# Kernel optimization log

Measured on AMD Instinct MI355X. Metric: run time of the kernel, lower is better.

## Reference

```python
import jax, jax.numpy as jnp
import numpy as np

B, S, HID = 2, 1024, 2048
NH, NKV = 32, 8
HD = HID // NH          # 64
N_REP = NH // NKV       # 4
ROPE_BASE = 10000.0


def rope_tables(seq_len, dim):
    inv_freq = 1.0 / (ROPE_BASE ** (np.arange(0, dim, 2, dtype=np.float32) / dim))
    t = jnp.arange(seq_len, dtype=jnp.float32)
    freqs = jnp.outer(t, jnp.asarray(inv_freq))          # [S, HD/2]
    emb = jnp.concatenate([freqs, freqs], axis=-1)       # [S, HD]
    return jnp.cos(emb), jnp.sin(emb)


def rotate_half(x):
    half = x.shape[-1] // 2
    return jnp.concatenate([-x[..., half:], x[..., :half]], axis=-1)


def setup_inputs() -> dict:
    key = jax.random.key(0)
    k1, k2, k3, k4, k5 = jax.random.split(key, 5)
    hidden_states = jax.random.normal(k1, (B, S, HID), dtype=jnp.float32)
    position_ids = jnp.broadcast_to(jnp.arange(S, dtype=jnp.int32), (B, S))
    # additive causal mask [B,1,S,S]: 0 where allowed, large negative where masked
    neg = jnp.finfo(jnp.float32).min
    causal = jnp.tril(jnp.ones((S, S), dtype=bool))
    attention_mask = jnp.where(causal, 0.0, neg)[None, None].astype(jnp.float32)
    attention_mask = jnp.broadcast_to(attention_mask, (B, 1, S, S))
    scale = 0.02
    Wq = jax.random.normal(k2, (HID, NH * HD), dtype=jnp.float32) * scale
    Wk = jax.random.normal(k3, (HID, NKV * HD), dtype=jnp.float32) * scale
    Wv = jax.random.normal(k4, (HID, NKV * HD), dtype=jnp.float32) * scale
    Wo = jax.random.normal(k5, (HID, HID), dtype=jnp.float32) * scale
    return {"hidden_states": hidden_states, "position_ids": position_ids,
            "attention_mask": attention_mask, "Wq": Wq, "Wk": Wk, "Wv": Wv, "Wo": Wo}


def reference(hidden_states, position_ids, attention_mask, Wq, Wk, Wv, Wo):
    b, s, _ = hidden_states.shape
    q = (hidden_states @ Wq).reshape(b, s, NH, HD).transpose(0, 2, 1, 3)    # [b,H,s,d]
    k = (hidden_states @ Wk).reshape(b, s, NKV, HD).transpose(0, 2, 1, 3)   # [b,kv,s,d]
    v = (hidden_states @ Wv).reshape(b, s, NKV, HD).transpose(0, 2, 1, 3)

    cos_t, sin_t = rope_tables(s, HD)                    # [s, d]
    cos = cos_t[position_ids][:, None]                   # [b,1,s,d]
    sin = sin_t[position_ids][:, None]
    q = q * cos + rotate_half(q) * sin
    k = k * cos + rotate_half(k) * sin

    # GQA: repeat each kv head N_REP times along the head axis
    k = jnp.repeat(k, N_REP, axis=1)                     # [b,H,s,d]
    v = jnp.repeat(v, N_REP, axis=1)

    scale = 1.0 / jnp.sqrt(jnp.asarray(HD, dtype=q.dtype))
    scores = jnp.einsum('bhqd,bhkd->bhqk', q, k) * scale
    scores = scores + attention_mask
    scores = jnp.maximum(scores, jnp.finfo(scores.dtype).min)
    w = jax.nn.softmax(scores, axis=-1)
    out = jnp.einsum('bhqk,bhkd->bhqd', w, v)            # [b,H,s,d]
    out = out.transpose(0, 2, 1, 3).reshape(b, s, HID)
    return out @ Wo
```

## Files before the change

kernel.cpp:

```cpp
#include <hip/hip_runtime.h>
#include <hip/hip_bf16.h>
#include <math.h>

constexpr int BB   = 2;
constexpr int SS   = 1024;
constexpr int HID  = 2048;
constexpr int NH   = 32;
constexpr int NKV  = 8;
constexpr int HD   = 64;
constexpr int M    = BB * SS;
constexpr int NQKV = 3072;

typedef __attribute__((ext_vector_type(8))) short bf8v;
typedef __attribute__((ext_vector_type(4))) float f4v;

static __device__ __forceinline__ unsigned short f2b(float x) {
  __hip_bfloat16 h = __float2bfloat16(x);
  return *reinterpret_cast<unsigned short*>(&h);
}
static __device__ __forceinline__ void gload16(void* lds, const void* g) {
  __builtin_amdgcn_global_load_lds(
      (const __attribute__((address_space(1))) void*)g,
      (__attribute__((address_space(3))) void*)lds, 16, 0, 0);
}

__global__ __launch_bounds__(256) void prepAll(
    const float* __restrict__ Wq, const float* __restrict__ Wk,
    const float* __restrict__ Wv, const float* __restrict__ Wo,
    const float* __restrict__ hidden, const int* __restrict__ pos_ids,
    unsigned short* __restrict__ WqkvT, unsigned short* __restrict__ WoT,
    unsigned short* __restrict__ Xb, float2* __restrict__ tab) {
  const int z = blockIdx.z;
  const int t = threadIdx.x;

  if (z == 4) {
    const int idx = blockIdx.y * 32 + blockIdx.x;
    if ((t & 127) < 32) {
      const int m = idx * 2 + (t >> 7);
      const int j = t & 31;
      const float pos = (float)pos_ids[m];
      const float ang = pos * exp2f(-(float)j * (13.287712379549449f / 32.0f));
      float sn, cs;
      sincosf(ang, &sn, &cs);
      tab[(size_t)m * 32 + j] = make_float2(cs, sn);
    }
    return;
  }
  if (z == 5) {
    const size_t base = ((size_t)(blockIdx.y * 32 + blockIdx.x)) * 4096;
#pragma unroll
    for (int it = 0; it < 2; ++it) {
      const size_t i = base + it * 2048 + t * 8;
      const float4 v0 = *(const float4*)(hidden + i);
      const float4 v1 = *(const float4*)(hidden + i + 4);
      unsigned short o[8] = {f2b(v0.x), f2b(v0.y), f2b(v0.z), f2b(v0.w),
                             f2b(v1.x), f2b(v1.y), f2b(v1.z), f2b(v1.w)};
      *(bf8v*)(Xb + i) = *(bf8v*)o;
    }
    return;
  }

  const float* src;
  unsigned short* dst;
  int C;
  if (z == 0)      { src = Wq; dst = WqkvT;                      C = 2048; }
  else if (z == 1) { src = Wk; dst = WqkvT + (size_t)2048 * HID; C = 512;  }
  else if (z == 2) { src = Wv; dst = WqkvT + (size_t)2560 * HID; C = 512;  }
  else             { src = Wo; dst = WoT;                        C = 2048; }

  const int r0 = blockIdx.y * 64, c0 = blockIdx.x * 64;
  if (c0 >= C) return;
  __shared__ float T[64][65];
  {
    const int r  = t >> 2;
    const int c4 = (t & 3) * 16;
    const float* sp = src + (size_t)(r0 + r) * C + c0 + c4;
    *(float4*)&T[r][c4 + 0]  = *(const float4*)(sp + 0);
    *(float4*)&T[r][c4 + 4]  = *(const float4*)(sp + 4);
    *(float4*)&T[r][c4 + 8]  = *(const float4*)(sp + 8);
    *(float4*)&T[r][c4 + 12] = *(const float4*)(sp + 12);
  }
  __syncthreads();
  {
    const int c  = t >> 2;
    const int rr = (t & 3) * 16;
    unsigned short o[16];
#pragma unroll
    for (int i = 0; i < 16; ++i) o[i] = f2b(T[rr + i][c]);
    unsigned short* dp = dst + (size_t)(c0 + c) * HID + r0 + rr;
    *(bf8v*)dp       = *(bf8v*)&o[0];
    *(bf8v*)(dp + 8) = *(bf8v*)&o[8];
  }
}

__global__ __launch_bounds__(256) void gemm_qkv(
    const unsigned short* __restrict__ A, const unsigned short* __restrict__ Bt,
    const float2* __restrict__ tab,
    unsigned short* __restrict__ Qb, unsigned short* __restrict__ Kb,
    unsigned short* __restrict__ Vb) {
  __shared__ unsigned short As[2][128 * 32];
  __shared__ unsigned short Bs[2][128 * 32];
  const int Kdim = HID;
  const int t  = threadIdx.x;
  const int w  = t >> 6, l = t & 63;
  const int lr = l & 15, lg = l >> 4;
  const int wr = w >> 1, wc = w & 1;
  const int bm = blockIdx.y * 128, bn = blockIdx.x * 128;

  f4v acc[4][4] = {};

  const unsigned short* Ablk = A  + (size_t)bm * Kdim;
  const unsigned short* Bblk = Bt + (size_t)bn * Kdim;
  const int srow = l >> 2;
  const int scol = (l & 3) * 8;

  auto stage = [&](int buf, int k0) {
    gload16(&As[buf][(w * 32)      * 32], Ablk + (size_t)(w * 32 +      srow) * Kdim + k0 + scol);
    gload16(&As[buf][(w * 32 + 16) * 32], Ablk + (size_t)(w * 32 + 16 + srow) * Kdim + k0 + scol);
    gload16(&Bs[buf][(w * 32)      * 32], Bblk + (size_t)(w * 32 +      srow) * Kdim + k0 + scol);
    gload16(&Bs[buf][(w * 32 + 16) * 32], Bblk + (size_t)(w * 32 + 16 + srow) * Kdim + k0 + scol);
  };

  stage(0, 0);
  __syncthreads();
  int cur = 0;
  for (int k0 = 0; k0 < Kdim; k0 += 32) {
    if (k0 + 32 < Kdim) stage(cur ^ 1, k0 + 32);

    bf8v aF[4], bF[4];
#pragma unroll
    for (int i = 0; i < 4; ++i) {
      aF[i] = *(const bf8v*)&As[cur][(wr * 64 + i * 16 + lr) * 32 + lg * 8];
      bF[i] = *(const bf8v*)&Bs[cur][(wc * 64 + i * 16 + lr) * 32 + lg * 8];
    }
    __builtin_amdgcn_s_setprio(1);
#pragma unroll
    for (int mi = 0; mi < 4; ++mi)
#pragma unroll
      for (int ni = 0; ni < 4; ++ni)
        acc[mi][ni] = __builtin_amdgcn_mfma_f32_16x16x32_bf16(aF[mi], bF[ni], acc[mi][ni], 0, 0, 0);
    __builtin_amdgcn_s_setprio(0);

    __syncthreads();
    cur ^= 1;
  }

  const int row0 = bm + wr * 64;
  const int colHead = bn + wc * 64;
  unsigned short* outArr;
  int hh, headsPerB, mode;
  if (colHead < 2048)      { mode = 0; outArr = Qb; hh = colHead >> 6;          headsPerB = NH;  }
  else if (colHead < 2560) { mode = 1; outArr = Kb; hh = (colHead - 2048) >> 6; headsPerB = NKV; }
  else                     { mode = 2; outArr = Vb; hh = (colHead - 2560) >> 6; headsPerB = NKV; }

#pragma unroll
  for (int mi = 0; mi < 4; ++mi)
#pragma unroll
    for (int r = 0; r < 4; ++r) {
      const int rowg = row0 + mi * 16 + lg * 4 + r;
      const int bI = rowg >> 10, s = rowg & (SS - 1);
      unsigned short* dst =
          outArr + ((size_t)(bI * headsPerB + hh) * SS + s) * 64;
      if (mode == 2) {
#pragma unroll
        for (int ni = 0; ni < 4; ++ni)
          dst[ni * 16 + lr] = f2b(acc[mi][ni][r]);
      } else {
        const float2 cs_lo = tab[(size_t)rowg * 32 + lr];
        const float2 cs_hi = tab[(size_t)rowg * 32 + 16 + lr];
#pragma unroll
        for (int ni = 0; ni < 4; ++ni) {
          const float2 cs = (ni & 1) ? cs_hi : cs_lo;
          const float x   = acc[mi][ni][r];
          const float prt = acc[mi][ni ^ 2][r];
          const float rh  = (ni < 2) ? -prt : prt;
          float v = x * cs.x + rh * cs.y;
          if (mode == 0) v *= 0.125f;
          dst[ni * 16 + lr] = f2b(v);
        }
      }
    }
}

__global__ __launch_bounds__(256) void gemm_bf16(
    const unsigned short* __restrict__ A, const unsigned short* __restrict__ Bt,
    float* __restrict__ C, int Ndim, int Kdim) {
  __shared__ unsigned short As[2][128 * 32];
  __shared__ unsigned short Bs[2][128 * 32];
  const int t  = threadIdx.x;
  const int w  = t >> 6, l = t & 63;
  const int lr = l & 15, lg = l >> 4;
  const int wr = w >> 1, wc = w & 1;
  const int bm = blockIdx.y * 128, bn = blockIdx.x * 128;

  f4v acc[4][4] = {};

  const unsigned short* Ablk = A  + (size_t)bm * Kdim;
  const unsigned short* Bblk = Bt + (size_t)bn * Kdim;
  const int srow = l >> 2;
  const int scol = (l & 3) * 8;

  auto stage = [&](int buf, int k0) {
    gload16(&As[buf][(w * 32)      * 32], Ablk + (size_t)(w * 32 +      srow) * Kdim + k0 + scol);
    gload16(&As[buf][(w * 32 + 16) * 32], Ablk + (size_t)(w * 32 + 16 + srow) * Kdim + k0 + scol);
    gload16(&Bs[buf][(w * 32)      * 32], Bblk + (size_t)(w * 32 +      srow) * Kdim + k0 + scol);
    gload16(&Bs[buf][(w * 32 + 16) * 32], Bblk + (size_t)(w * 32 + 16 + srow) * Kdim + k0 + scol);
  };

  stage(0, 0);
  __syncthreads();
  int cur = 0;
  for (int k0 = 0; k0 < Kdim; k0 += 32) {
    if (k0 + 32 < Kdim) stage(cur ^ 1, k0 + 32);

    bf8v aF[4], bF[4];
#pragma unroll
    for (int i = 0; i < 4; ++i) {
      aF[i] = *(const bf8v*)&As[cur][(wr * 64 + i * 16 + lr) * 32 + lg * 8];
      bF[i] = *(const bf8v*)&Bs[cur][(wc * 64 + i * 16 + lr) * 32 + lg * 8];
    }
    __builtin_amdgcn_s_setprio(1);
#pragma unroll
    for (int mi = 0; mi < 4; ++mi)
#pragma unroll
      for (int ni = 0; ni < 4; ++ni)
        acc[mi][ni] = __builtin_amdgcn_mfma_f32_16x16x32_bf16(aF[mi], bF[ni], acc[mi][ni], 0, 0, 0);
    __builtin_amdgcn_s_setprio(0);

    __syncthreads();
    cur ^= 1;
  }

  const int row0 = bm + wr * 64;
  const int col0 = bn + wc * 64;
#pragma unroll
  for (int mi = 0; mi < 4; ++mi)
#pragma unroll
    for (int r = 0; r < 4; ++r) {
      const size_t rowoff = (size_t)(row0 + mi * 16 + lg * 4 + r) * Ndim;
#pragma unroll
      for (int ni = 0; ni < 4; ++ni)
        C[rowoff + col0 + ni * 16 + lr] = acc[mi][ni][r];
    }
}

__global__ __launch_bounds__(256) void vtrans(
    const unsigned short* __restrict__ Vb, unsigned short* __restrict__ Vt) {
  const int bkv = blockIdx.y;
  const int s0  = blockIdx.x * 64;
  __shared__ unsigned short T[64][72];
  const int t = threadIdx.x;
  const unsigned short* src = Vb + ((size_t)bkv * SS + s0) * 64;
  {
    const int r  = t >> 2;
    const int co = (t & 3) * 16;
    *(bf8v*)&T[r][co]     = *(const bf8v*)(src + (size_t)r * 64 + co);
    *(bf8v*)&T[r][co + 8] = *(const bf8v*)(src + (size_t)r * 64 + co + 8);
  }
  __syncthreads();
  {
    const int d  = t >> 2;
    const int so = (t & 3) * 16;
    unsigned short tmp[16];
#pragma unroll
    for (int i = 0; i < 16; ++i) tmp[i] = T[so + i][d];
    unsigned short* dst = Vt + ((size_t)(bkv * 64 + d)) * SS + s0 + so;
    *(bf8v*)dst       = *(bf8v*)&tmp[0];
    *(bf8v*)(dst + 8) = *(bf8v*)&tmp[8];
  }
}

__global__ __launch_bounds__(128) void attn_mfma(
    const unsigned short* __restrict__ Qb, const unsigned short* __restrict__ Kb,
    const unsigned short* __restrict__ Vt, unsigned short* __restrict__ attn) {
  const int xb = blockIdx.x;
  const int h = blockIdx.y, b = blockIdx.z;
  const int kv = h >> 2;
  const int w  = threadIdx.x >> 6;
  const int l  = threadIdx.x & 63;
  const int lr = l & 15;
  const int lg = l >> 4;
  const int t  = threadIdx.x;

  __shared__ unsigned short VT[64][72];
  __shared__ unsigned short PL[2][16][72];

  const unsigned short* Kp = Kb + ((size_t)((b * NKV + kv) * SS)) * 64;
  const unsigned short* Vp = Vt + ((size_t)((b * NKV + kv) * 64)) * SS;

  const int vd  = t >> 1;
  const int vso = (t & 1) * 32;

  for (int half = 0; half < 2; ++half) {
    const int qt = half ? (31 - xb) : xb;
    const int qbase = qt * 32;
    const int qW = qbase + w * 16;
    const unsigned short* Qp = Qb + ((size_t)((b * NH + h) * SS + qW)) * 64;
    bf8v aQ0 = *(const bf8v*)(Qp + (size_t)lr * 64 + lg * 8);
    bf8v aQ1 = *(const bf8v*)(Qp + (size_t)lr * 64 + 32 + lg * 8);

    f4v o[4] = {{0,0,0,0},{0,0,0,0},{0,0,0,0},{0,0,0,0}};
    float lsumL[4] = {0.f, 0.f, 0.f, 0.f};

    for (int kvb = 0; kvb < qbase + 32; kvb += 64) {
      __syncthreads();
      const unsigned short* vp = Vp + (size_t)vd * SS + kvb + vso;
      const bf8v v0 = *(const bf8v*)(vp);
      const bf8v v1 = *(const bf8v*)(vp + 8);
      const bf8v v2 = *(const bf8v*)(vp + 16);
      const bf8v v3 = *(const bf8v*)(vp + 24);

      f4v sc[4] = {{0,0,0,0},{0,0,0,0},{0,0,0,0},{0,0,0,0}};
      __builtin_amdgcn_s_setprio(1);
#pragma unroll
      for (int c = 0; c < 4; ++c) {
        const unsigned short* kr = Kp + (size_t)(kvb + c * 16 + lr) * 64 + lg * 8;
        bf8v b0 = *(const bf8v*)(kr);
        bf8v b1 = *(const bf8v*)(kr + 32);
        sc[c] = __builtin_amdgcn_mfma_f32_16x16x32_bf16(aQ0, b0, sc[c], 0, 0, 0);
        sc[c] = __builtin_amdgcn_mfma_f32_16x16x32_bf16(aQ1, b1, sc[c], 0, 0, 0);
      }
      __builtin_amdgcn_s_setprio(0);

#pragma unroll
      for (int r = 0; r < 4; ++r) {
        const int qrow = qW + lg * 4 + r;
        float ps = 0.f;
        unsigned short pb[4];
#pragma unroll
        for (int c = 0; c < 4; ++c) {
          const float s = ((kvb + c * 16 + lr) > qrow) ? -INFINITY : sc[c][r];
          const float p = __expf(s);
          ps += p;
          pb[c] = f2b(p);
        }
        lsumL[r] += ps;
#pragma unroll
        for (int c = 0; c < 4; ++c) PL[w][lg * 4 + r][c * 16 + lr] = pb[c];
      }

      *(bf8v*)&VT[vd][vso]      = v0;
      *(bf8v*)&VT[vd][vso + 8]  = v1;
      *(bf8v*)&VT[vd][vso + 16] = v2;
      *(bf8v*)&VT[vd][vso + 24] = v3;

      __syncthreads();

      bf8v aP0 = *(const bf8v*)&PL[w][lr][lg * 8];
      bf8v aP1 = *(const bf8v*)&PL[w][lr][32 + lg * 8];
      __builtin_amdgcn_s_setprio(1);
#pragma unroll
      for (int n = 0; n < 4; ++n) {
        bf8v bV0 = *(const bf8v*)&VT[n * 16 + lr][lg * 8];
        bf8v bV1 = *(const bf8v*)&VT[n * 16 + lr][32 + lg * 8];
        o[n] = __builtin_amdgcn_mfma_f32_16x16x32_bf16(aP0, bV0, o[n], 0, 0, 0);
        o[n] = __builtin_amdgcn_mfma_f32_16x16x32_bf16(aP1, bV1, o[n], 0, 0, 0);
      }
      __builtin_amdgcn_s_setprio(0);
    }

#pragma unroll
    for (int r = 0; r < 4; ++r) {
      float ls = lsumL[r];
      ls += __shfl_xor(ls, 1);
      ls += __shfl_xor(ls, 2);
      ls += __shfl_xor(ls, 4);
      ls += __shfl_xor(ls, 8);
      const float inv = 1.0f / ls;
      const int row = qW + lg * 4 + r;
      unsigned short* dst = attn + (size_t)(b * SS + row) * HID + h * 64;
#pragma unroll
      for (int n = 0; n < 4; ++n) dst[n * 16 + lr] = f2b(o[n][r] * inv);
    }
  }
}

extern "C" void kernel_launch(void* const* d_in, const int* in_sizes, int n_in,
                              void* d_out, int out_size, void* d_ws, size_t ws_size,
                              hipStream_t stream) {
  const float* hidden = (const float*)d_in[0];
  const int*   pos    = (const int*)d_in[1];
  const float* Wq = (const float*)d_in[3];
  const float* Wk = (const float*)d_in[4];
  const float* Wv = (const float*)d_in[5];
  const float* Wo = (const float*)d_in[6];
  float* out = (float*)d_out;

  char* ws = (char*)d_ws;
  unsigned short* WqkvT = (unsigned short*)(ws);
  unsigned short* WoT   = (unsigned short*)(ws + 12582912);
  unsigned short* Xb    = (unsigned short*)(ws + 20971520);
  unsigned short* attnb = Xb;
  unsigned short* Qb    = (unsigned short*)(ws + 29360128);
  unsigned short* Kb    = (unsigned short*)(ws + 37748736);
  unsigned short* Vb    = (unsigned short*)(ws + 39845888);
  unsigned short* Vt    = (unsigned short*)(ws + 41943040);
  float2*         tab   = (float2*)(ws + 44040192);

  dim3 blk(256);

  prepAll<<<dim3(32, 32, 6), blk, 0, stream>>>(Wq, Wk, Wv, Wo, hidden, pos,
                                               WqkvT, WoT, Xb, tab);

  gemm_qkv<<<dim3(NQKV / 128, M / 128), blk, 0, stream>>>(Xb, WqkvT, tab, Qb, Kb, Vb);

  vtrans<<<dim3(SS / 64, BB * NKV), blk, 0, stream>>>(Vb, Vt);

  attn_mfma<<<dim3(16, NH, BB), dim3(128), 0, stream>>>(Qb, Kb, Vt, attnb);

  gemm_bf16<<<dim3(HID / 128, M / 128), blk, 0, stream>>>(attnb, WoT, out, HID, HID);
}
```

Baseline: 162.8 us.

## Triple-buffer GEMM LDS staging with partial vmcnt waits and XOR swizzle

```diff
diff --git a/kernel.cpp b/kernel.cpp
--- a/kernel.cpp
+++ b/kernel.cpp
@@ -93,13 +93,14 @@
   }
 }
 
+
 __global__ __launch_bounds__(256) void gemm_qkv(
     const unsigned short* __restrict__ A, const unsigned short* __restrict__ Bt,
     const float2* __restrict__ tab,
     unsigned short* __restrict__ Qb, unsigned short* __restrict__ Kb,
     unsigned short* __restrict__ Vb) {
-  __shared__ unsigned short As[2][128 * 32];
-  __shared__ unsigned short Bs[2][128 * 32];
+  __shared__ unsigned short As[3][128 * 32];
+  __shared__ unsigned short Bs[3][128 * 32];
   const int Kdim = HID;
   const int t  = threadIdx.x;
   const int w  = t >> 6, l = t & 63;
@@ -112,7 +113,8 @@
   const unsigned short* Ablk = A  + (size_t)bm * Kdim;
   const unsigned short* Bblk = Bt + (size_t)bn * Kdim;
   const int srow = l >> 2;
-  const int scol = (l & 3) * 8;
+  const int scol = (((l & 3) ^ ((srow >> 1) & 3)) * 8);
+  const int rsl  = (lg ^ ((lr >> 1) & 3)) * 8;
 
   auto stage = [&](int buf, int k0) {
     gload16(&As[buf][(w * 32)      * 32], Ablk + (size_t)(w * 32 +      srow) * Kdim + k0 + scol);
@@ -121,17 +123,23 @@
     gload16(&Bs[buf][(w * 32 + 16) * 32], Bblk + (size_t)(w * 32 + 16 + srow) * Kdim + k0 + scol);
   };
 
+  const int nsteps = Kdim / 32;
   stage(0, 0);
-  __syncthreads();
+  stage(1, 32);
+  asm volatile("s_waitcnt vmcnt(4)" ::: "memory");
+  __builtin_amdgcn_s_barrier();
+
   int cur = 0;
-  for (int k0 = 0; k0 < Kdim; k0 += 32) {
-    if (k0 + 32 < Kdim) stage(cur ^ 1, k0 + 32);
+  const int aoff = (wr * 64 + lr) * 32 + rsl;
+  const int boff = (wc * 64 + lr) * 32 + rsl;
+  for (int tt = 0; tt < nsteps; ++tt) {
+    if (tt + 2 < nsteps) stage((tt + 2) % 3, (tt + 2) * 32);
 
     bf8v aF[4], bF[4];
 #pragma unroll
     for (int i = 0; i < 4; ++i) {
-      aF[i] = *(const bf8v*)&As[cur][(wr * 64 + i * 16 + lr) * 32 + lg * 8];
-      bF[i] = *(const bf8v*)&Bs[cur][(wc * 64 + i * 16 + lr) * 32 + lg * 8];
+      aF[i] = *(const bf8v*)&As[cur][aoff + i * 512];
+      bF[i] = *(const bf8v*)&Bs[cur][boff + i * 512];
     }
     __builtin_amdgcn_s_setprio(1);
 #pragma unroll
@@ -141,8 +149,10 @@
         acc[mi][ni] = __builtin_amdgcn_mfma_f32_16x16x32_bf16(aF[mi], bF[ni], acc[mi][ni], 0, 0, 0);
     __builtin_amdgcn_s_setprio(0);
 
-    __syncthreads();
-    cur ^= 1;
+    if (tt + 2 < nsteps) { asm volatile("s_waitcnt vmcnt(4)" ::: "memory"); }
+    else                 { asm volatile("s_waitcnt vmcnt(0)" ::: "memory"); }
+    __builtin_amdgcn_s_barrier();
+    cur = (cur + 1) % 3;
   }
 
   const int row0 = bm + wr * 64;
@@ -185,8 +195,8 @@
 __global__ __launch_bounds__(256) void gemm_bf16(
     const unsigned short* __restrict__ A, const unsigned short* __restrict__ Bt,
     float* __restrict__ C, int Ndim, int Kdim) {
-  __shared__ unsigned short As[2][128 * 32];
-  __shared__ unsigned short Bs[2][128 * 32];
+  __shared__ unsigned short As[3][128 * 32];
+  __shared__ unsigned short Bs[3][128 * 32];
   const int t  = threadIdx.x;
   const int w  = t >> 6, l = t & 63;
   const int lr = l & 15, lg = l >> 4;
@@ -198,7 +208,8 @@
   const unsigned short* Ablk = A  + (size_t)bm * Kdim;
   const unsigned short* Bblk = Bt + (size_t)bn * Kdim;
   const int srow = l >> 2;
-  const int scol = (l & 3) * 8;
+  const int scol = (((l & 3) ^ ((srow >> 1) & 3)) * 8);
+  const int rsl  = (lg ^ ((lr >> 1) & 3)) * 8;
 
   auto stage = [&](int buf, int k0) {
     gload16(&As[buf][(w * 32)      * 32], Ablk + (size_t)(w * 32 +      srow) * Kdim + k0 + scol);
@@ -207,17 +218,23 @@
     gload16(&Bs[buf][(w * 32 + 16) * 32], Bblk + (size_t)(w * 32 + 16 + srow) * Kdim + k0 + scol);
   };
 
+  const int nsteps = Kdim / 32;
   stage(0, 0);
-  __syncthreads();
+  stage(1, 32);
+  asm volatile("s_waitcnt vmcnt(4)" ::: "memory");
+  __builtin_amdgcn_s_barrier();
+
   int cur = 0;
-  for (int k0 = 0; k0 < Kdim; k0 += 32) {
-    if (k0 + 32 < Kdim) stage(cur ^ 1, k0 + 32);
+  const int aoff = (wr * 64 + lr) * 32 + rsl;
+  const int boff = (wc * 64 + lr) * 32 + rsl;
+  for (int tt = 0; tt < nsteps; ++tt) {
+    if (tt + 2 < nsteps) stage((tt + 2) % 3, (tt + 2) * 32);
 
     bf8v aF[4], bF[4];
 #pragma unroll
     for (int i = 0; i < 4; ++i) {
-      aF[i] = *(const bf8v*)&As[cur][(wr * 64 + i * 16 + lr) * 32 + lg * 8];
-      bF[i] = *(const bf8v*)&Bs[cur][(wc * 64 + i * 16 + lr) * 32 + lg * 8];
+      aF[i] = *(const bf8v*)&As[cur][aoff + i * 512];
+      bF[i] = *(const bf8v*)&Bs[cur][boff + i * 512];
     }
     __builtin_amdgcn_s_setprio(1);
 #pragma unroll
@@ -227,8 +244,10 @@
         acc[mi][ni] = __builtin_amdgcn_mfma_f32_16x16x32_bf16(aF[mi], bF[ni], acc[mi][ni], 0, 0, 0);
     __builtin_amdgcn_s_setprio(0);
 
-    __syncthreads();
-    cur ^= 1;
+    if (tt + 2 < nsteps) { asm volatile("s_waitcnt vmcnt(4)" ::: "memory"); }
+    else                 { asm volatile("s_waitcnt vmcnt(0)" ::: "memory"); }
+    __builtin_amdgcn_s_barrier();
+    cur = (cur + 1) % 3;
   }
 
   const int row0 = bm + wr * 64;
```

Result: slower. 175.2 us (+7.7%).
